# Kernel optimization log

Hardware: AMD Instinct MI355X
Metric: run time of the kernel (lower is better)

## Reference

```python
import jax, jax.numpy as jnp
import numpy as np

N = 16384       # structure nodes
H = 256         # in_channels == hidden_channels
E_BOLD = 524288
E_TEMP = 262144
T_ATTR = 107    # hardcoded in temporal_edge_proj Linear(107, hidden)
EPS = 1e-5


def layer_norm(x, g, b):
    m = x.mean(-1, keepdims=True)
    v = ((x - m) ** 2).mean(-1, keepdims=True)
    return (x - m) * jax.lax.rsqrt(v + EPS) * g + b


def gcn_conv(x, W, b, edge_index, edge_weight):
    """PyG GCNConv: add self-loops (weight 1), symmetric normalization,
    out_i = sum_j norm_ij * (x_j @ W) + b."""
    n = x.shape[0]
    loop = jnp.arange(n)
    row = jnp.concatenate([edge_index[0], loop])   # source
    col = jnp.concatenate([edge_index[1], loop])   # target
    w = jnp.concatenate([edge_weight, jnp.ones((n,), x.dtype)])
    deg = jax.ops.segment_sum(w, col, num_segments=n)
    dis = jnp.where(deg > 0, jax.lax.rsqrt(jnp.where(deg > 0, deg, 1.0)), 0.0)
    norm = dis[row] * w * dis[col]
    h = x @ W                                       # [n, H]
    out = jax.ops.segment_sum(norm[:, None] * h[row], col, num_segments=n)
    return out + b


def setup_inputs() -> dict:
    key = jax.random.key(0)
    ks = jax.random.split(key, 12)
    s = 1.0 / np.sqrt(H)
    return {
        "x_struct": jax.random.normal(ks[0], (N, H), jnp.float32),
        "bold_edge_index": jax.random.randint(ks[1], (2, E_BOLD), 0, N),
        "bold_edge_weight": jax.random.uniform(ks[2], (E_BOLD,), jnp.float32),
        "temp_edge_index": jax.random.randint(ks[3], (2, E_TEMP), 0, N),
        "temp_edge_attr": jax.random.normal(ks[4], (E_TEMP, T_ATTR), jnp.float32),
        "W_bold": jax.random.normal(ks[5], (H, H), jnp.float32) * s,
        "b_bold": jnp.zeros((H,), jnp.float32),
        "W_temp": jax.random.normal(ks[6], (H, H), jnp.float32) * s,
        "b_temp": jnp.zeros((H,), jnp.float32),
        "ln_struct_g": jnp.ones((H,), jnp.float32),
        "ln_struct_b": jnp.zeros((H,), jnp.float32),
        "ln_temp_g": jnp.ones((H,), jnp.float32),
        "ln_temp_b": jnp.zeros((H,), jnp.float32),
        "proj_w1": jax.random.normal(ks[7], (T_ATTR, H), jnp.float32) / np.sqrt(T_ATTR),
        "proj_b1": jnp.zeros((H,), jnp.float32),
        "proj_g": jnp.ones((H,), jnp.float32),
        "proj_beta": jnp.zeros((H,), jnp.float32),
        "proj_w2": jax.random.normal(ks[8], (H, 1), jnp.float32) * 0.01,
        "proj_b2": jnp.ones((1,), jnp.float32),  # keeps temporal edge weights > 0 (valid GCN norm)
    }


def reference(x_struct, bold_edge_index, bold_edge_weight, temp_edge_index,
              temp_edge_attr, W_bold, b_bold, W_temp, b_temp,
              ln_struct_g, ln_struct_b, ln_temp_g, ln_temp_b,
              proj_w1, proj_b1, proj_g, proj_beta, proj_w2, proj_b2):
    s0 = x_struct
    # bold GCN + residual + struct_norm + relu
    bold_out = gcn_conv(s0, W_bold, b_bold, bold_edge_index, bold_edge_weight)
    s = jax.nn.relu(layer_norm(bold_out + s0, ln_struct_g, ln_struct_b))
    # temporal edge-attr MLP -> scalar edge weight (temporal_dim == 1)
    h = jax.nn.relu(layer_norm(temp_edge_attr @ proj_w1 + proj_b1, proj_g, proj_beta))
    temp_w = (h @ proj_w2 + proj_b2)[:, 0]          # [E_TEMP]
    # temporal GCN + residual + temporal_norm + relu
    temporal_out = gcn_conv(s, W_temp, b_temp, temp_edge_index, temp_w)
    s = jax.nn.relu(layer_norm(temporal_out + s, ln_temp_g, ln_temp_b))
    # final residual to original features through struct_norm
    return layer_norm(s + s0, ln_struct_g, ln_struct_b)
```

## Files before the change

### kernel.cpp

```cpp
#include <hip/hip_runtime.h>

constexpr int kN  = 16384;
constexpr int kEB = 524288;
constexpr int kET = 262144;
constexpr int kTA = 107;
constexpr float kEps = 1e-5f;
#define HN 256

typedef __attribute__((ext_vector_type(8))) short short8;
typedef __attribute__((ext_vector_type(4))) float floatx4;
typedef unsigned short u16;
typedef unsigned int u32;

#define GLOAD_LDS16(gp, lp)                                                    \
  __builtin_amdgcn_global_load_lds(                                            \
      (const __attribute__((address_space(1))) u32*)(gp),                      \
      (__attribute__((address_space(3))) u32*)(lp), 16, 0, 0)

__device__ __forceinline__ u32 bf16rn(float f) {
  u32 u = __float_as_uint(f);
  return (u + 0x7FFFu + ((u >> 16) & 1u)) >> 16;
}
__device__ __forceinline__ u32 pack2(float a, float b) {
  return bf16rn(a) | (bf16rn(b) << 16);
}
__device__ __forceinline__ float bf2f(u32 v) {
  return __uint_as_float(v << 16);
}
__device__ __forceinline__ u32 cvtpk(float lo, float hi) {
  u32 r;
  asm("v_cvt_pk_bf16_f32 %0, %1, %2" : "=v"(r) : "v"(lo), "v"(hi));
  return r;
}
__device__ __forceinline__ void ub8(uint4 u, float* f) {
  f[0] = bf2f(u.x & 0xFFFF); f[1] = bf2f(u.x >> 16);
  f[2] = bf2f(u.y & 0xFFFF); f[3] = bf2f(u.y >> 16);
  f[4] = bf2f(u.z & 0xFFFF); f[5] = bf2f(u.z >> 16);
  f[6] = bf2f(u.w & 0xFFFF); f[7] = bf2f(u.w >> 16);
}
__device__ __forceinline__ u32 swz512(u32 b) { return b ^ (((b >> 9) & 7u) << 4); }

__global__ __launch_bounds__(256)
void k_pack(const float* __restrict__ w1, const float* __restrict__ Wb,
            const float* __restrict__ Wt, const float* __restrict__ b1,
            const float* __restrict__ pg, const float* __restrict__ pbeta,
            const float* __restrict__ w2, u16* __restrict__ pk1,
            u16* __restrict__ pkb, u16* __restrict__ pkt,
            float4* __restrict__ pp) {
  int idx = blockIdx.x * 256 + threadIdx.x;
  if (idx < 32768) {
    int e = idx & 7, lane = (idx >> 3) & 63, ct = (idx >> 9) & 15, kk = idx >> 13;
    int k = kk * 32 + (lane >> 4) * 8 + e, col = ct * 16 + (lane & 15);
    pk1[idx] = (u16)(k < kTA ? bf16rn(w1[(size_t)k * 256 + col]) : 0);
  } else if (idx < 163840) {
    int j = idx - 32768;
    const float* W = (j < 65536) ? Wb : Wt;
    u16* pk = (j < 65536) ? pkb : pkt;
    int t = j & 65535;
    int e = t & 7, lane = (t >> 3) & 63, ct = (t >> 9) & 15, kt = t >> 13;
    int k = kt * 32 + (lane >> 4) * 8 + e, col = ct * 16 + (lane & 15);
    pk[t] = (u16)bf16rn(W[(size_t)k * 256 + col]);
  } else if (idx < 163840 + 256) {
    int col = idx - 163840;
    pp[col] = make_float4(b1[col], pg[col], pbeta[col], w2[col]);
  }
}

__global__ __launch_bounds__(256)
void k_cvt(const float* __restrict__ in, u16* __restrict__ out) {
  size_t i = (size_t)(blockIdx.x * 256 + threadIdx.x) * 8;
  float4 a = *(const float4*)(in + i);
  float4 b = *(const float4*)(in + i + 4);
  uint4 o = make_uint4(pack2(a.x, a.y), pack2(a.z, a.w),
                       pack2(b.x, b.y), pack2(b.z, b.w));
  *(uint4*)(out + i) = o;
}

__global__ __launch_bounds__(256)
void k_edge_prep_both(const int* __restrict__ bcol, const float* __restrict__ bw,
                      const int* __restrict__ tcol, const float* __restrict__ tw,
                      float* __restrict__ deg_b, int* __restrict__ cnt_b,
                      float* __restrict__ deg_t, int* __restrict__ cnt_t) {
  int e = blockIdx.x * 256 + threadIdx.x;
  if (e < kEB) {
    int c = bcol[e];
    atomicAdd(&deg_b[c], bw[e]);
    atomicAdd(&cnt_b[c], 1);
  } else {
    int t = e - kEB;
    int c = tcol[t];
    atomicAdd(&deg_t[c], tw[t]);
    atomicAdd(&cnt_t[c], 1);
  }
}

__global__ __launch_bounds__(256)
void k_scan_both(const int* __restrict__ cnt_b, int* __restrict__ base_b,
                 int* __restrict__ cur_b, const float* __restrict__ deg_b,
                 float* __restrict__ dis_b, const int* __restrict__ cnt_t,
                 int* __restrict__ base_t, int* __restrict__ cur_t,
                 const float* __restrict__ deg_t, float* __restrict__ dis_t) {
  const int* cnt = blockIdx.x ? cnt_t : cnt_b;
  int* base = blockIdx.x ? base_t : base_b;
  int* cur  = blockIdx.x ? cur_t : cur_b;
  const float* deg = blockIdx.x ? deg_t : deg_b;
  float* dis = blockIdx.x ? dis_t : dis_b;
  __shared__ int part[256];
  int tid = threadIdx.x;
  int per = kN >> 8;
  int i0 = tid * per;
  int s = 0;
  for (int k = 0; k < per; ++k) s += cnt[i0 + k];
  part[tid] = s;
  __syncthreads();
  for (int off = 1; off < 256; off <<= 1) {
    int v = (tid >= off) ? part[tid - off] : 0;
    __syncthreads();
    part[tid] += v;
    __syncthreads();
  }
  int run = (tid == 0) ? 0 : part[tid - 1];
  for (int k = 0; k < per; ++k) {
    base[i0 + k] = run; cur[i0 + k] = run; run += cnt[i0 + k];
    float d = deg[i0 + k] + 1.0f;
    dis[i0 + k] = (d > 0.f) ? rsqrtf(d) : 0.f;
  }
  if (tid == 255) base[kN] = run;
}

__global__ __launch_bounds__(256)
void k_fill_both(const int* __restrict__ bei, const float* __restrict__ bw,
                 const float* __restrict__ dis_b, int* __restrict__ cur_b,
                 int2* __restrict__ csr_b, const int* __restrict__ tei,
                 const float* __restrict__ tw, const float* __restrict__ dis_t,
                 int* __restrict__ cur_t, int2* __restrict__ csr_t) {
  int e = blockIdx.x * 256 + threadIdx.x;
  if (e < kEB) {
    int r = bei[e], c = bei[kEB + e];
    float nrm = dis_b[r] * bw[e] * dis_b[c];
    int pos = atomicAdd(&cur_b[c], 1);
    csr_b[pos] = make_int2(r, __float_as_int(nrm));
  } else {
    int t = e - kEB;
    int r = tei[t], c = tei[kET + t];
    float nrm = dis_t[r] * tw[t] * dis_t[c];
    int pos = atomicAdd(&cur_t[c], 1);
    csr_t[pos] = make_int2(r, __float_as_int(nrm));
  }
}

__global__ __launch_bounds__(256)
void k_gemm_mfma(const u16* __restrict__ Ab, const u16* __restrict__ pkW,
                 u16* __restrict__ Cb) {
  __shared__ __align__(16) u16 Atile[32 * 256];
  int tid = threadIdx.x;
  int w = tid >> 6, lane = tid & 63, low4 = lane & 15, hi = lane >> 4;
  int row0 = blockIdx.x * 32;

  const char* asrc = (const char*)(Ab + (size_t)row0 * 256);
#pragma unroll
  for (int i = 0; i < 4; ++i) {
    u32 d = (u32)(((i * 4 + w) * 64 + lane) * 16);
    GLOAD_LDS16(asrc + swz512(d), (char*)Atile + (i * 4 + w) * 1024);
  }

  floatx4 acc[2][4];
#pragma unroll
  for (int rt = 0; rt < 2; ++rt)
#pragma unroll
    for (int nn = 0; nn < 4; ++nn) acc[rt][nn] = (floatx4){0.f, 0.f, 0.f, 0.f};

  __syncthreads();

#pragma unroll
  for (int kt = 0; kt < 8; ++kt) {
    short8 bfr[4];
    const u16* pw = pkW + ((size_t)(kt * 16 + w * 4) * 64 + lane) * 8;
#pragma unroll
    for (int nn = 0; nn < 4; ++nn) bfr[nn] = *(const short8*)(pw + nn * 512);
    short8 afr[2];
#pragma unroll
    for (int rt = 0; rt < 2; ++rt) {
      u32 p = (u32)((rt * 16 + low4) * 512 + (kt * 32 + hi * 8) * 2);
      afr[rt] = *(const short8*)((const char*)Atile + swz512(p));
    }
#pragma unroll
    for (int rt = 0; rt < 2; ++rt)
#pragma unroll
      for (int nn = 0; nn < 4; ++nn)
        acc[rt][nn] = __builtin_amdgcn_mfma_f32_16x16x32_bf16(afr[rt], bfr[nn],
                                                              acc[rt][nn], 0, 0, 0);
  }
#pragma unroll
  for (int rt = 0; rt < 2; ++rt)
#pragma unroll
    for (int nn = 0; nn < 4; ++nn)
#pragma unroll
      for (int j = 0; j < 4; ++j) {
        int row = row0 + rt * 16 + hi * 4 + j;
        int col = w * 64 + nn * 16 + low4;
        Cb[(size_t)row * 256 + col] = (u16)bf16rn(acc[rt][nn][j]);
      }
}

#define PROJ_TILES 4
__global__ __launch_bounds__(512)
void k_proj_mfma(const float* __restrict__ attr, const u16* __restrict__ pk1,
                 const float* __restrict__ b1, const float4* __restrict__ pp,
                 const float* __restrict__ b2, float* __restrict__ temp_w) {
  __shared__ __align__(16) u16 Btile[32768];
  int tid = threadIdx.x;
  int w = tid >> 6, lane = tid & 63, low4 = lane & 15, hi = lane >> 4;

#pragma unroll
  for (int it = 0; it < 8; ++it) {
    int chunk = it * 512 + tid;
    GLOAD_LDS16((const char*)pk1 + (size_t)chunk * 16,
                (char*)Btile + (it * 512 + w * 64) * 16);
  }

  auto buildA = [&](int t, short8* a) {
    int e0 = (blockIdx.x * PROJ_TILES + t) * 128 + w * 16;
    const float* rowp = attr + (size_t)(e0 + low4) * kTA;
#pragma unroll
    for (int kk = 0; kk < 4; ++kk) {
      int kb = kk * 32 + hi * 8;
      float v[8];
#pragma unroll
      for (int e = 0; e < 8; ++e)
        v[e] = (kk < 3 || kb + e < kTA) ? rowp[kb + e] : 0.f;
      union { short8 s8; uint4 u4; } fr;
      fr.u4 = make_uint4(cvtpk(v[0], v[1]), cvtpk(v[2], v[3]),
                         cvtpk(v[4], v[5]), cvtpk(v[6], v[7]));
      a[kk] = fr.s8;
    }
  };

  short8 a_cur[4];
  buildA(0, a_cur);
  float b2s = b2[0];

  __syncthreads();

#pragma unroll
  for (int t = 0; t < PROJ_TILES; ++t) {
    int e0 = (blockIdx.x * PROJ_TILES + t) * 128 + w * 16;

    short8 a_next[4];
    if (t + 1 < PROJ_TILES) buildA(t + 1, a_next);

    u32 hvpk[16][2];
    float s1[4] = {0.f, 0.f, 0.f, 0.f}, s2[4] = {0.f, 0.f, 0.f, 0.f};
#pragma unroll
    for (int nn = 0; nn < 16; ++nn) {
      floatx4 acc = (floatx4){0.f, 0.f, 0.f, 0.f};
#pragma unroll
      for (int kk = 0; kk < 4; ++kk) {
        short8 bfr = *(const short8*)(Btile + ((size_t)(kk * 16 + nn) * 64 + lane) * 8);
        acc = __builtin_amdgcn_mfma_f32_16x16x32_bf16(a_cur[kk], bfr, acc, 0, 0, 0);
      }
      float b1v = b1[nn * 16 + low4];
      float h0 = acc[0] + b1v, h1 = acc[1] + b1v, h2 = acc[2] + b1v, h3 = acc[3] + b1v;
      s1[0] += h0; s2[0] += h0 * h0;
      s1[1] += h1; s2[1] += h1 * h1;
      s1[2] += h2; s2[2] += h2 * h2;
      s1[3] += h3; s2[3] += h3 * h3;
      hvpk[nn][0] = cvtpk(h0, h1);
      hvpk[nn][1] = cvtpk(h2, h3);
    }

    float mean[4], inv[4];
#pragma unroll
    for (int j = 0; j < 4; ++j) {
#pragma unroll
      for (int m = 1; m < 16; m <<= 1) {
        s1[j] += __shfl_xor(s1[j], m, 64);
        s2[j] += __shfl_xor(s2[j], m, 64);
      }
      mean[j] = s1[j] * (1.f / 256);
      inv[j] = rsqrtf(s2[j] * (1.f / 256) - mean[j] * mean[j] + kEps);
    }

    float d[4] = {0.f, 0.f, 0.f, 0.f};
#pragma unroll
    for (int nn = 0; nn < 16; ++nn) {
      float4 p = pp[nn * 16 + low4];
      float h0 = bf2f(hvpk[nn][0] & 0xFFFF);
      float h1 = bf2f(hvpk[nn][0] >> 16);
      float h2 = bf2f(hvpk[nn][1] & 0xFFFF);
      float h3 = bf2f(hvpk[nn][1] >> 16);
      d[0] += fmaxf((h0 - mean[0]) * inv[0] * p.y + p.z, 0.f) * p.w;
      d[1] += fmaxf((h1 - mean[1]) * inv[1] * p.y + p.z, 0.f) * p.w;
      d[2] += fmaxf((h2 - mean[2]) * inv[2] * p.y + p.z, 0.f) * p.w;
      d[3] += fmaxf((h3 - mean[3]) * inv[3] * p.y + p.z, 0.f) * p.w;
    }
#pragma unroll
    for (int j = 0; j < 4; ++j) {
#pragma unroll
      for (int m = 1; m < 16; m <<= 1) d[j] += __shfl_xor(d[j], m, 64);
      if (low4 == 0) temp_w[e0 + hi * 4 + j] = d[j] + b2s;
    }

#pragma unroll
    for (int kk = 0; kk < 4; ++kk) a_cur[kk] = a_next[kk];
  }
}

template <int FINAL>
__global__ __launch_bounds__(256)
void k_agg_ln(const u16* __restrict__ h, const void* __restrict__ residv,
              const float* __restrict__ x0, const int2* __restrict__ csr,
              const int* __restrict__ basep, const float* __restrict__ dis,
              const float* __restrict__ bias, const float* __restrict__ g1,
              const float* __restrict__ b1, const float* __restrict__ g2,
              const float* __restrict__ b2, void* __restrict__ outv) {
  int tid = threadIdx.x;
  int sub = tid >> 5, lane = tid & 31;
  int node = blockIdx.x * 8 + sub;
  int c = lane * 8;
  const u16* hcol = h + c;
  float di = dis[node];
  float sl = di * di;
  float acc[8];
  {
    uint4 u = *(const uint4*)(hcol + (size_t)node * HN);
    float f[8]; ub8(u, f);
#pragma unroll
    for (int i = 0; i < 8; ++i) acc[i] = f[i] * sl;
  }
  int e0 = basep[node], e1 = basep[node + 1];
  int k = e0;
  for (; k + 4 <= e1; k += 4) {
    int2 p0 = csr[k], p1 = csr[k + 1], p2 = csr[k + 2], p3 = csr[k + 3];
    uint4 u0 = *(const uint4*)(hcol + (size_t)p0.x * HN);
    uint4 u1 = *(const uint4*)(hcol + (size_t)p1.x * HN);
    uint4 u2 = *(const uint4*)(hcol + (size_t)p2.x * HN);
    uint4 u3 = *(const uint4*)(hcol + (size_t)p3.x * HN);
    float n0 = __int_as_float(p0.y), n1 = __int_as_float(p1.y);
    float n2 = __int_as_float(p2.y), n3 = __int_as_float(p3.y);
    float f0[8], f1[8], f2[8], f3[8];
    ub8(u0, f0); ub8(u1, f1); ub8(u2, f2); ub8(u3, f3);
#pragma unroll
    for (int i = 0; i < 8; ++i)
      acc[i] += n0 * f0[i] + n1 * f1[i] + n2 * f2[i] + n3 * f3[i];
  }
  for (; k < e1; ++k) {
    int2 p = csr[k];
    uint4 u = *(const uint4*)(hcol + (size_t)p.x * HN);
    float nf = __int_as_float(p.y);
    float f[8]; ub8(u, f);
#pragma unroll
    for (int i = 0; i < 8; ++i) acc[i] += nf * f[i];
  }
  float v[8];
  {
    float4 b0 = *(const float4*)(bias + c);
    float4 b4 = *(const float4*)(bias + c + 4);
    float bb[8] = {b0.x, b0.y, b0.z, b0.w, b4.x, b4.y, b4.z, b4.w};
    float rr[8];
    if (!FINAL) {
      const float* rp = (const float*)residv + (size_t)node * HN + c;
      float4 r0 = *(const float4*)rp;
      float4 r4 = *(const float4*)(rp + 4);
      rr[0] = r0.x; rr[1] = r0.y; rr[2] = r0.z; rr[3] = r0.w;
      rr[4] = r4.x; rr[5] = r4.y; rr[6] = r4.z; rr[7] = r4.w;
    } else {
      uint4 u = *(const uint4*)((const u16*)residv + (size_t)node * HN + c);
      ub8(u, rr);
    }
#pragma unroll
    for (int i = 0; i < 8; ++i) v[i] = acc[i] + bb[i] + rr[i];
  }
  float s1 = 0.f, s2 = 0.f;
#pragma unroll
  for (int i = 0; i < 8; ++i) { s1 += v[i]; s2 += v[i] * v[i]; }
#pragma unroll
  for (int m = 1; m < 32; m <<= 1) {
    s1 += __shfl_xor(s1, m, 64);
    s2 += __shfl_xor(s2, m, 64);
  }
  float mean = s1 * (1.f / HN);
  float inv = rsqrtf(s2 * (1.f / HN) - mean * mean + kEps);
  float4 ga = *(const float4*)(g1 + c);
  float4 gb = *(const float4*)(g1 + c + 4);
  float4 ba = *(const float4*)(b1 + c);
  float4 bbv = *(const float4*)(b1 + c + 4);
  float gg[8] = {ga.x, ga.y, ga.z, ga.w, gb.x, gb.y, gb.z, gb.w};
  float bt[8] = {ba.x, ba.y, ba.z, ba.w, bbv.x, bbv.y, bbv.z, bbv.w};
  float y[8];
#pragma unroll
  for (int i = 0; i < 8; ++i)
    y[i] = fmaxf((v[i] - mean) * inv * gg[i] + bt[i], 0.f);
  if (!FINAL) {
    uint4 o = make_uint4(cvtpk(y[0], y[1]), cvtpk(y[2], y[3]),
                         cvtpk(y[4], y[5]), cvtpk(y[6], y[7]));
    *(uint4*)((u16*)outv + (size_t)node * HN + c) = o;
  } else {
    const float* xp = x0 + (size_t)node * HN + c;
    float4 x0v = *(const float4*)xp;
    float4 x4v = *(const float4*)(xp + 4);
    float xx[8] = {x0v.x, x0v.y, x0v.z, x0v.w, x4v.x, x4v.y, x4v.z, x4v.w};
    float z[8];
    float t1 = 0.f, t2 = 0.f;
#pragma unroll
    for (int i = 0; i < 8; ++i) {
      z[i] = y[i] + xx[i];
      t1 += z[i]; t2 += z[i] * z[i];
    }
#pragma unroll
    for (int m = 1; m < 32; m <<= 1) {
      t1 += __shfl_xor(t1, m, 64);
      t2 += __shfl_xor(t2, m, 64);
    }
    float m2 = t1 * (1.f / HN);
    float i2 = rsqrtf(t2 * (1.f / HN) - m2 * m2 + kEps);
    float4 Ga = *(const float4*)(g2 + c);
    float4 Gb = *(const float4*)(g2 + c + 4);
    float4 Ba = *(const float4*)(b2 + c);
    float4 Bb = *(const float4*)(b2 + c + 4);
    float G[8] = {Ga.x, Ga.y, Ga.z, Ga.w, Gb.x, Gb.y, Gb.z, Gb.w};
    float B[8] = {Ba.x, Ba.y, Ba.z, Ba.w, Bb.x, Bb.y, Bb.z, Bb.w};
    float* op = (float*)outv + (size_t)node * HN + c;
    float4 o0 = make_float4((z[0] - m2) * i2 * G[0] + B[0],
                            (z[1] - m2) * i2 * G[1] + B[1],
                            (z[2] - m2) * i2 * G[2] + B[2],
                            (z[3] - m2) * i2 * G[3] + B[3]);
    float4 o4 = make_float4((z[4] - m2) * i2 * G[4] + B[4],
                            (z[5] - m2) * i2 * G[5] + B[5],
                            (z[6] - m2) * i2 * G[6] + B[6],
                            (z[7] - m2) * i2 * G[7] + B[7]);
    *(float4*)op = o0;
    *(float4*)(op + 4) = o4;
  }
}

extern "C" void kernel_launch(void* const* d_in, const int* in_sizes, int n_in,
                              void* d_out, int out_size, void* d_ws, size_t ws_size,
                              hipStream_t stream) {
  const float* x     = (const float*)d_in[0];
  const int*   bei   = (const int*)d_in[1];
  const float* bew   = (const float*)d_in[2];
  const int*   tei   = (const int*)d_in[3];
  const float* tattr = (const float*)d_in[4];
  const float* Wb    = (const float*)d_in[5];
  const float* bb    = (const float*)d_in[6];
  const float* Wt    = (const float*)d_in[7];
  const float* bt    = (const float*)d_in[8];
  const float* gs    = (const float*)d_in[9];
  const float* bs    = (const float*)d_in[10];
  const float* gt    = (const float*)d_in[11];
  const float* btn   = (const float*)d_in[12];
  const float* pw1   = (const float*)d_in[13];
  const float* pb1   = (const float*)d_in[14];
  const float* pg    = (const float*)d_in[15];
  const float* pbeta = (const float*)d_in[16];
  const float* pw2   = (const float*)d_in[17];
  const float* pb2   = (const float*)d_in[18];
  float* outp = (float*)d_out;

  size_t off = 0;
  auto alloc = [&](size_t bytes) -> void* {
    void* p = (char*)d_ws + off;
    off += (bytes + 255) & ~(size_t)255;
    return p;
  };
  float* deg_b = (float*)alloc(kN * 4);
  float* deg_t = (float*)alloc(kN * 4);
  int*   cnt_b = (int*)alloc(kN * 4);
  int*   cnt_t = (int*)alloc(kN * 4);
  float* dis_b = (float*)alloc(kN * 4);
  float* dis_t = (float*)alloc(kN * 4);
  int*   base_b = (int*)alloc((kN + 1) * 4);
  int*   base_t = (int*)alloc((kN + 1) * 4);
  int*   cur_b  = (int*)alloc(kN * 4);
  int*   cur_t  = (int*)alloc(kN * 4);
  float* tmpw   = (float*)alloc(kET * 4);
  int2*  csr_b  = (int2*)alloc((size_t)kEB * 8);
  int2*  csr_t  = (int2*)alloc((size_t)kET * 8);
  u16*   pk1 = (u16*)alloc(32768 * 2);
  u16*   pkb = (u16*)alloc(65536 * 2);
  u16*   pkt = (u16*)alloc(65536 * 2);
  float4* pp = (float4*)alloc(256 * 16);
  u16*   xb  = (u16*)alloc((size_t)kN * HN * 2);
  u16*   hb  = (u16*)alloc((size_t)kN * HN * 2);
  u16*   sb  = (u16*)alloc((size_t)kN * HN * 2);
  (void)ws_size; (void)in_sizes; (void)n_in; (void)out_size;

  hipMemsetAsync(deg_b, 0, (size_t)4 * kN * 4, stream);

  k_pack<<<641, 256, 0, stream>>>(pw1, Wb, Wt, pb1, pg, pbeta, pw2,
                                  pk1, pkb, pkt, pp);
  k_cvt<<<kN * HN / 8 / 256, 256, 0, stream>>>(x, xb);

  k_proj_mfma<<<kET / 128 / PROJ_TILES, 512, 0, stream>>>(tattr, pk1, pb1, pp,
                                                          pb2, tmpw);

  k_edge_prep_both<<<(kEB + kET) / 256, 256, 0, stream>>>(
      bei + kEB, bew, tei + kET, tmpw, deg_b, cnt_b, deg_t, cnt_t);
  k_scan_both<<<2, 256, 0, stream>>>(cnt_b, base_b, cur_b, deg_b, dis_b,
                                     cnt_t, base_t, cur_t, deg_t, dis_t);
  k_fill_both<<<(kEB + kET) / 256, 256, 0, stream>>>(
      bei, bew, dis_b, cur_b, csr_b, tei, tmpw, dis_t, cur_t, csr_t);

  k_gemm_mfma<<<kN / 32, 256, 0, stream>>>(xb, pkb, hb);
  k_agg_ln<0><<<kN / 8, 256, 0, stream>>>(hb, x, nullptr, csr_b, base_b, dis_b,
                                          bb, gs, bs, nullptr, nullptr, sb);
  k_gemm_mfma<<<kN / 32, 256, 0, stream>>>(sb, pkt, hb);
  k_agg_ln<1><<<kN / 8, 256, 0, stream>>>(hb, sb, x, csr_t, base_t, dis_t,
                                          bt, gt, btn, gs, bs, outp);
}
```

Before: 270.4 us.

## Fuse independent stages into horizontally merged kernels to cut launches and overlap work

```diff
diff --git a/kernel.cpp b/kernel.cpp
--- a/kernel.cpp
+++ b/kernel.cpp
@@ -41,70 +41,202 @@
 __device__ __forceinline__ u32 swz512(u32 b) { return b ^ (((b >> 9) & 7u) << 4); }
 
 __global__ __launch_bounds__(256)
-void k_pack(const float* __restrict__ w1, const float* __restrict__ Wb,
-            const float* __restrict__ Wt, const float* __restrict__ b1,
-            const float* __restrict__ pg, const float* __restrict__ pbeta,
-            const float* __restrict__ w2, u16* __restrict__ pk1,
-            u16* __restrict__ pkb, u16* __restrict__ pkt,
-            float4* __restrict__ pp) {
-  int idx = blockIdx.x * 256 + threadIdx.x;
-  if (idx < 32768) {
-    int e = idx & 7, lane = (idx >> 3) & 63, ct = (idx >> 9) & 15, kk = idx >> 13;
-    int k = kk * 32 + (lane >> 4) * 8 + e, col = ct * 16 + (lane & 15);
-    pk1[idx] = (u16)(k < kTA ? bf16rn(w1[(size_t)k * 256 + col]) : 0);
-  } else if (idx < 163840) {
-    int j = idx - 32768;
-    const float* W = (j < 65536) ? Wb : Wt;
-    u16* pk = (j < 65536) ? pkb : pkt;
-    int t = j & 65535;
-    int e = t & 7, lane = (t >> 3) & 63, ct = (t >> 9) & 15, kt = t >> 13;
-    int k = kt * 32 + (lane >> 4) * 8 + e, col = ct * 16 + (lane & 15);
-    pk[t] = (u16)bf16rn(W[(size_t)k * 256 + col]);
-  } else if (idx < 163840 + 256) {
-    int col = idx - 163840;
-    pp[col] = make_float4(b1[col], pg[col], pbeta[col], w2[col]);
-  }
-}
-
-__global__ __launch_bounds__(256)
-void k_cvt(const float* __restrict__ in, u16* __restrict__ out) {
-  size_t i = (size_t)(blockIdx.x * 256 + threadIdx.x) * 8;
-  float4 a = *(const float4*)(in + i);
-  float4 b = *(const float4*)(in + i + 4);
-  uint4 o = make_uint4(pack2(a.x, a.y), pack2(a.z, a.w),
-                       pack2(b.x, b.y), pack2(b.z, b.w));
-  *(uint4*)(out + i) = o;
-}
-
-__global__ __launch_bounds__(256)
-void k_edge_prep_both(const int* __restrict__ bcol, const float* __restrict__ bw,
-                      const int* __restrict__ tcol, const float* __restrict__ tw,
-                      float* __restrict__ deg_b, int* __restrict__ cnt_b,
-                      float* __restrict__ deg_t, int* __restrict__ cnt_t) {
-  int e = blockIdx.x * 256 + threadIdx.x;
-  if (e < kEB) {
-    int c = bcol[e];
-    atomicAdd(&deg_b[c], bw[e]);
-    atomicAdd(&cnt_b[c], 1);
+void k_prep_const(const float* __restrict__ w1, const float* __restrict__ Wb,
+                  const float* __restrict__ Wt, const float* __restrict__ b1,
+                  const float* __restrict__ pg, const float* __restrict__ pbeta,
+                  const float* __restrict__ w2, u16* __restrict__ pk1,
+                  u16* __restrict__ pkb, u16* __restrict__ pkt,
+                  float4* __restrict__ pp, const float* __restrict__ x,
+                  u16* __restrict__ xb, uint4* __restrict__ zero4) {
+  int bid = blockIdx.x, tid = threadIdx.x;
+  if (bid < 641) {
+    int idx = bid * 256 + tid;
+    if (idx < 32768) {
+      int e = idx & 7, lane = (idx >> 3) & 63, ct = (idx >> 9) & 15, kk = idx >> 13;
+      int k = kk * 32 + (lane >> 4) * 8 + e, col = ct * 16 + (lane & 15);
+      pk1[idx] = (u16)(k < kTA ? bf16rn(w1[(size_t)k * 256 + col]) : 0);
+    } else if (idx < 163840) {
+      int j = idx - 32768;
+      const float* W = (j < 65536) ? Wb : Wt;
+      u16* pk = (j < 65536) ? pkb : pkt;
+      int t = j & 65535;
+      int e = t & 7, lane = (t >> 3) & 63, ct = (t >> 9) & 15, kt = t >> 13;
+      int k = kt * 32 + (lane >> 4) * 8 + e, col = ct * 16 + (lane & 15);
+      pk[t] = (u16)bf16rn(W[(size_t)k * 256 + col]);
+    } else if (idx < 163840 + 256) {
+      int col = idx - 163840;
+      pp[col] = make_float4(b1[col], pg[col], pbeta[col], w2[col]);
+    }
+  } else if (bid < 641 + 2048) {
+    size_t i = (size_t)((bid - 641) * 256 + tid) * 8;
+    float4 a = *(const float4*)(x + i);
+    float4 b = *(const float4*)(x + i + 4);
+    *(uint4*)(xb + i) = make_uint4(pack2(a.x, a.y), pack2(a.z, a.w),
+                                   pack2(b.x, b.y), pack2(b.z, b.w));
   } else {
-    int t = e - kEB;
-    int c = tcol[t];
-    atomicAdd(&deg_t[c], tw[t]);
-    atomicAdd(&cnt_t[c], 1);
-  }
-}
-
-__global__ __launch_bounds__(256)
-void k_scan_both(const int* __restrict__ cnt_b, int* __restrict__ base_b,
-                 int* __restrict__ cur_b, const float* __restrict__ deg_b,
-                 float* __restrict__ dis_b, const int* __restrict__ cnt_t,
-                 int* __restrict__ base_t, int* __restrict__ cur_t,
-                 const float* __restrict__ deg_t, float* __restrict__ dis_t) {
-  const int* cnt = blockIdx.x ? cnt_t : cnt_b;
-  int* base = blockIdx.x ? base_t : base_b;
-  int* cur  = blockIdx.x ? cur_t : cur_b;
-  const float* deg = blockIdx.x ? deg_t : deg_b;
-  float* dis = blockIdx.x ? dis_t : dis_b;
+    zero4[(bid - 2689) * 256 + tid] = make_uint4(0, 0, 0, 0);
+  }
+}
+
+#define PROJ_TILES 4
+__device__ __forceinline__
+void proj_role(u16* Btile, const float* __restrict__ attr,
+               const u16* __restrict__ pk1, const float* __restrict__ b1,
+               const float4* __restrict__ pp, const float* __restrict__ b2,
+               float* __restrict__ temp_w, int projid, int tid) {
+  int w = tid >> 6, lane = tid & 63, low4 = lane & 15, hi = lane >> 4;
+
+#pragma unroll
+  for (int it = 0; it < 8; ++it) {
+    int chunk = it * 512 + tid;
+    GLOAD_LDS16((const char*)pk1 + (size_t)chunk * 16,
+                (char*)Btile + (it * 512 + w * 64) * 16);
+  }
+
+  auto buildA = [&](int t, short8* a) {
+    int e0 = (projid * PROJ_TILES + t) * 128 + w * 16;
+    const float* rowp = attr + (size_t)(e0 + low4) * kTA;
+#pragma unroll
+    for (int kk = 0; kk < 4; ++kk) {
+      int kb = kk * 32 + hi * 8;
+      float v[8];
+#pragma unroll
+      for (int e = 0; e < 8; ++e)
+        v[e] = (kk < 3 || kb + e < kTA) ? rowp[kb + e] : 0.f;
+      union { short8 s8; uint4 u4; } fr;
+      fr.u4 = make_uint4(cvtpk(v[0], v[1]), cvtpk(v[2], v[3]),
+                         cvtpk(v[4], v[5]), cvtpk(v[6], v[7]));
+      a[kk] = fr.s8;
+    }
+  };
+
+  short8 a_cur[4];
+  buildA(0, a_cur);
+  float b2s = b2[0];
+
+  __syncthreads();
+
+#pragma unroll
+  for (int t = 0; t < PROJ_TILES; ++t) {
+    int e0 = (projid * PROJ_TILES + t) * 128 + w * 16;
+    short8 a_next[4];
+    if (t + 1 < PROJ_TILES) buildA(t + 1, a_next);
+
+    u32 hvpk[16][2];
+    float s1[4] = {0.f, 0.f, 0.f, 0.f}, s2[4] = {0.f, 0.f, 0.f, 0.f};
+#pragma unroll
+    for (int nn = 0; nn < 16; ++nn) {
+      floatx4 acc = (floatx4){0.f, 0.f, 0.f, 0.f};
+#pragma unroll
+      for (int kk = 0; kk < 4; ++kk) {
+        short8 bfr = *(const short8*)(Btile + ((size_t)(kk * 16 + nn) * 64 + lane) * 8);
+        acc = __builtin_amdgcn_mfma_f32_16x16x32_bf16(a_cur[kk], bfr, acc, 0, 0, 0);
+      }
+      float b1v = b1[nn * 16 + low4];
+      float h0 = acc[0] + b1v, h1 = acc[1] + b1v, h2 = acc[2] + b1v, h3 = acc[3] + b1v;
+      s1[0] += h0; s2[0] += h0 * h0;
+      s1[1] += h1; s2[1] += h1 * h1;
+      s1[2] += h2; s2[2] += h2 * h2;
+      s1[3] += h3; s2[3] += h3 * h3;
+      hvpk[nn][0] = cvtpk(h0, h1);
+      hvpk[nn][1] = cvtpk(h2, h3);
+    }
+
+    float mean[4], inv[4];
+#pragma unroll
+    for (int j = 0; j < 4; ++j) {
+#pragma unroll
+      for (int m = 1; m < 16; m <<= 1) {
+        s1[j] += __shfl_xor(s1[j], m, 64);
+        s2[j] += __shfl_xor(s2[j], m, 64);
+      }
+      mean[j] = s1[j] * (1.f / 256);
+      inv[j] = rsqrtf(s2[j] * (1.f / 256) - mean[j] * mean[j] + kEps);
+    }
+
+    float d[4] = {0.f, 0.f, 0.f, 0.f};
+#pragma unroll
+    for (int nn = 0; nn < 16; ++nn) {
+      float4 p = pp[nn * 16 + low4];
+      float h0 = bf2f(hvpk[nn][0] & 0xFFFF);
+      float h1 = bf2f(hvpk[nn][0] >> 16);
+      float h2 = bf2f(hvpk[nn][1] & 0xFFFF);
+      float h3 = bf2f(hvpk[nn][1] >> 16);
+      d[0] += fmaxf((h0 - mean[0]) * inv[0] * p.y + p.z, 0.f) * p.w;
+      d[1] += fmaxf((h1 - mean[1]) * inv[1] * p.y + p.z, 0.f) * p.w;
+      d[2] += fmaxf((h2 - mean[2]) * inv[2] * p.y + p.z, 0.f) * p.w;
+      d[3] += fmaxf((h3 - mean[3]) * inv[3] * p.y + p.z, 0.f) * p.w;
+    }
+#pragma unroll
+    for (int j = 0; j < 4; ++j) {
+#pragma unroll
+      for (int m = 1; m < 16; m <<= 1) d[j] += __shfl_xor(d[j], m, 64);
+      if (low4 == 0) temp_w[e0 + hi * 4 + j] = d[j] + b2s;
+    }
+#pragma unroll
+    for (int kk = 0; kk < 4; ++kk) a_cur[kk] = a_next[kk];
+  }
+}
+
+__device__ __forceinline__
+void gemm64_role(u16* shmem, const u16* __restrict__ Ab,
+                 const u16* __restrict__ pkW, u16* __restrict__ Cb,
+                 int gid, int tid) {
+  int half = tid >> 8, t = tid & 255;
+  int w = t >> 6, lane = t & 63, low4 = lane & 15, hi = lane >> 4;
+  int row0 = gid * 64 + half * 32;
+  u16* Atile = shmem + half * 8192;
+
+  const char* asrc = (const char*)(Ab + (size_t)row0 * 256);
+#pragma unroll
+  for (int i = 0; i < 4; ++i) {
+    u32 d = (u32)(((i * 4 + w) * 64 + lane) * 16);
+    GLOAD_LDS16(asrc + swz512(d), (char*)Atile + (i * 4 + w) * 1024);
+  }
+
+  floatx4 acc[2][4];
+#pragma unroll
+  for (int rt = 0; rt < 2; ++rt)
+#pragma unroll
+    for (int nn = 0; nn < 4; ++nn) acc[rt][nn] = (floatx4){0.f, 0.f, 0.f, 0.f};
+
+  __syncthreads();
+
+#pragma unroll
+  for (int kt = 0; kt < 8; ++kt) {
+    short8 bfr[4];
+    const u16* pw = pkW + ((size_t)(kt * 16 + w * 4) * 64 + lane) * 8;
+#pragma unroll
+    for (int nn = 0; nn < 4; ++nn) bfr[nn] = *(const short8*)(pw + nn * 512);
+    short8 afr[2];
+#pragma unroll
+    for (int rt = 0; rt < 2; ++rt) {
+      u32 p = (u32)((rt * 16 + low4) * 512 + (kt * 32 + hi * 8) * 2);
+      afr[rt] = *(const short8*)((const char*)Atile + swz512(p));
+    }
+#pragma unroll
+    for (int rt = 0; rt < 2; ++rt)
+#pragma unroll
+      for (int nn = 0; nn < 4; ++nn)
+        acc[rt][nn] = __builtin_amdgcn_mfma_f32_16x16x32_bf16(afr[rt], bfr[nn],
+                                                              acc[rt][nn], 0, 0, 0);
+  }
+#pragma unroll
+  for (int rt = 0; rt < 2; ++rt)
+#pragma unroll
+    for (int nn = 0; nn < 4; ++nn)
+#pragma unroll
+      for (int j = 0; j < 4; ++j) {
+        int row = row0 + rt * 16 + hi * 4 + j;
+        int col = w * 64 + nn * 16 + low4;
+        Cb[(size_t)row * 256 + col] = (u16)bf16rn(acc[rt][nn][j]);
+      }
+}
+
+__device__ __forceinline__
+void scan_role(const int* __restrict__ cnt, int* __restrict__ base,
+               int* __restrict__ cur, const float* __restrict__ deg,
+               float* __restrict__ dis) {
   __shared__ int part[256];
   int tid = threadIdx.x;
   int per = kN >> 8;
@@ -128,195 +260,17 @@
   if (tid == 255) base[kN] = run;
 }
 
-__global__ __launch_bounds__(256)
-void k_fill_both(const int* __restrict__ bei, const float* __restrict__ bw,
-                 const float* __restrict__ dis_b, int* __restrict__ cur_b,
-                 int2* __restrict__ csr_b, const int* __restrict__ tei,
-                 const float* __restrict__ tw, const float* __restrict__ dis_t,
-                 int* __restrict__ cur_t, int2* __restrict__ csr_t) {
-  int e = blockIdx.x * 256 + threadIdx.x;
-  if (e < kEB) {
-    int r = bei[e], c = bei[kEB + e];
-    float nrm = dis_b[r] * bw[e] * dis_b[c];
-    int pos = atomicAdd(&cur_b[c], 1);
-    csr_b[pos] = make_int2(r, __float_as_int(nrm));
-  } else {
-    int t = e - kEB;
-    int r = tei[t], c = tei[kET + t];
-    float nrm = dis_t[r] * tw[t] * dis_t[c];
-    int pos = atomicAdd(&cur_t[c], 1);
-    csr_t[pos] = make_int2(r, __float_as_int(nrm));
-  }
-}
-
-__global__ __launch_bounds__(256)
-void k_gemm_mfma(const u16* __restrict__ Ab, const u16* __restrict__ pkW,
-                 u16* __restrict__ Cb) {
-  __shared__ __align__(16) u16 Atile[32 * 256];
-  int tid = threadIdx.x;
-  int w = tid >> 6, lane = tid & 63, low4 = lane & 15, hi = lane >> 4;
-  int row0 = blockIdx.x * 32;
-
-  const char* asrc = (const char*)(Ab + (size_t)row0 * 256);
-#pragma unroll
-  for (int i = 0; i < 4; ++i) {
-    u32 d = (u32)(((i * 4 + w) * 64 + lane) * 16);
-    GLOAD_LDS16(asrc + swz512(d), (char*)Atile + (i * 4 + w) * 1024);
-  }
-
-  floatx4 acc[2][4];
-#pragma unroll
-  for (int rt = 0; rt < 2; ++rt)
-#pragma unroll
-    for (int nn = 0; nn < 4; ++nn) acc[rt][nn] = (floatx4){0.f, 0.f, 0.f, 0.f};
-
-  __syncthreads();
-
-#pragma unroll
-  for (int kt = 0; kt < 8; ++kt) {
-    short8 bfr[4];
-    const u16* pw = pkW + ((size_t)(kt * 16 + w * 4) * 64 + lane) * 8;
-#pragma unroll
-    for (int nn = 0; nn < 4; ++nn) bfr[nn] = *(const short8*)(pw + nn * 512);
-    short8 afr[2];
-#pragma unroll
-    for (int rt = 0; rt < 2; ++rt) {
-      u32 p = (u32)((rt * 16 + low4) * 512 + (kt * 32 + hi * 8) * 2);
-      afr[rt] = *(const short8*)((const char*)Atile + swz512(p));
-    }
-#pragma unroll
-    for (int rt = 0; rt < 2; ++rt)
-#pragma unroll
-      for (int nn = 0; nn < 4; ++nn)
-        acc[rt][nn] = __builtin_amdgcn_mfma_f32_16x16x32_bf16(afr[rt], bfr[nn],
-                                                              acc[rt][nn], 0, 0, 0);
-  }
-#pragma unroll
-  for (int rt = 0; rt < 2; ++rt)
-#pragma unroll
-    for (int nn = 0; nn < 4; ++nn)
-#pragma unroll
-      for (int j = 0; j < 4; ++j) {
-        int row = row0 + rt * 16 + hi * 4 + j;
-        int col = w * 64 + nn * 16 + low4;
-        Cb[(size_t)row * 256 + col] = (u16)bf16rn(acc[rt][nn][j]);
-      }
-}
-
-#define PROJ_TILES 4
-__global__ __launch_bounds__(512)
-void k_proj_mfma(const float* __restrict__ attr, const u16* __restrict__ pk1,
-                 const float* __restrict__ b1, const float4* __restrict__ pp,
-                 const float* __restrict__ b2, float* __restrict__ temp_w) {
-  __shared__ __align__(16) u16 Btile[32768];
-  int tid = threadIdx.x;
-  int w = tid >> 6, lane = tid & 63, low4 = lane & 15, hi = lane >> 4;
-
-#pragma unroll
-  for (int it = 0; it < 8; ++it) {
-    int chunk = it * 512 + tid;
-    GLOAD_LDS16((const char*)pk1 + (size_t)chunk * 16,
-                (char*)Btile + (it * 512 + w * 64) * 16);
-  }
-
-  auto buildA = [&](int t, short8* a) {
-    int e0 = (blockIdx.x * PROJ_TILES + t) * 128 + w * 16;
-    const float* rowp = attr + (size_t)(e0 + low4) * kTA;
-#pragma unroll
-    for (int kk = 0; kk < 4; ++kk) {
-      int kb = kk * 32 + hi * 8;
-      float v[8];
-#pragma unroll
-      for (int e = 0; e < 8; ++e)
-        v[e] = (kk < 3 || kb + e < kTA) ? rowp[kb + e] : 0.f;
-      union { short8 s8; uint4 u4; } fr;
-      fr.u4 = make_uint4(cvtpk(v[0], v[1]), cvtpk(v[2], v[3]),
-                         cvtpk(v[4], v[5]), cvtpk(v[6], v[7]));
-      a[kk] = fr.s8;
-    }
-  };
-
-  short8 a_cur[4];
-  buildA(0, a_cur);
-  float b2s = b2[0];
-
-  __syncthreads();
-
-#pragma unroll
-  for (int t = 0; t < PROJ_TILES; ++t) {
-    int e0 = (blockIdx.x * PROJ_TILES + t) * 128 + w * 16;
-
-    short8 a_next[4];
-    if (t + 1 < PROJ_TILES) buildA(t + 1, a_next);
-
-    u32 hvpk[16][2];
-    float s1[4] = {0.f, 0.f, 0.f, 0.f}, s2[4] = {0.f, 0.f, 0.f, 0.f};
-#pragma unroll
-    for (int nn = 0; nn < 16; ++nn) {
-      floatx4 acc = (floatx4){0.f, 0.f, 0.f, 0.f};
-#pragma unroll
-      for (int kk = 0; kk < 4; ++kk) {
-        short8 bfr = *(const short8*)(Btile + ((size_t)(kk * 16 + nn) * 64 + lane) * 8);
-        acc = __builtin_amdgcn_mfma_f32_16x16x32_bf16(a_cur[kk], bfr, acc, 0, 0, 0);
-      }
-      float b1v = b1[nn * 16 + low4];
-      float h0 = acc[0] + b1v, h1 = acc[1] + b1v, h2 = acc[2] + b1v, h3 = acc[3] + b1v;
-      s1[0] += h0; s2[0] += h0 * h0;
-      s1[1] += h1; s2[1] += h1 * h1;
-      s1[2] += h2; s2[2] += h2 * h2;
-      s1[3] += h3; s2[3] += h3 * h3;
-      hvpk[nn][0] = cvtpk(h0, h1);
-      hvpk[nn][1] = cvtpk(h2, h3);
-    }
-
-    float mean[4], inv[4];
-#pragma unroll
-    for (int j = 0; j < 4; ++j) {
-#pragma unroll
-      for (int m = 1; m < 16; m <<= 1) {
-        s1[j] += __shfl_xor(s1[j], m, 64);
-        s2[j] += __shfl_xor(s2[j], m, 64);
-      }
-      mean[j] = s1[j] * (1.f / 256);
-      inv[j] = rsqrtf(s2[j] * (1.f / 256) - mean[j] * mean[j] + kEps);
-    }
-
-    float d[4] = {0.f, 0.f, 0.f, 0.f};
-#pragma unroll
-    for (int nn = 0; nn < 16; ++nn) {
-      float4 p = pp[nn * 16 + low4];
-      float h0 = bf2f(hvpk[nn][0] & 0xFFFF);
-      float h1 = bf2f(hvpk[nn][0] >> 16);
-      float h2 = bf2f(hvpk[nn][1] & 0xFFFF);
-      float h3 = bf2f(hvpk[nn][1] >> 16);
-      d[0] += fmaxf((h0 - mean[0]) * inv[0] * p.y + p.z, 0.f) * p.w;
-      d[1] += fmaxf((h1 - mean[1]) * inv[1] * p.y + p.z, 0.f) * p.w;
-      d[2] += fmaxf((h2 - mean[2]) * inv[2] * p.y + p.z, 0.f) * p.w;
-      d[3] += fmaxf((h3 - mean[3]) * inv[3] * p.y + p.z, 0.f) * p.w;
-    }
-#pragma unroll
-    for (int j = 0; j < 4; ++j) {
-#pragma unroll
-      for (int m = 1; m < 16; m <<= 1) d[j] += __shfl_xor(d[j], m, 64);
-      if (low4 == 0) temp_w[e0 + hi * 4 + j] = d[j] + b2s;
-    }
-
-#pragma unroll
-    for (int kk = 0; kk < 4; ++kk) a_cur[kk] = a_next[kk];
-  }
-}
-
 template <int FINAL>
-__global__ __launch_bounds__(256)
-void k_agg_ln(const u16* __restrict__ h, const void* __restrict__ residv,
+__device__ __forceinline__
+void agg_role(const u16* __restrict__ h, const void* __restrict__ residv,
               const float* __restrict__ x0, const int2* __restrict__ csr,
               const int* __restrict__ basep, const float* __restrict__ dis,
               const float* __restrict__ bias, const float* __restrict__ g1,
               const float* __restrict__ b1, const float* __restrict__ g2,
-              const float* __restrict__ b2, void* __restrict__ outv) {
+              const float* __restrict__ b2, void* __restrict__ outv, int aid) {
   int tid = threadIdx.x;
   int sub = tid >> 5, lane = tid & 31;
-  int node = blockIdx.x * 8 + sub;
+  int node = aid * 8 + sub;
   int c = lane * 8;
   const u16* hcol = h + c;
   float di = dis[node];
@@ -421,17 +375,160 @@
     float G[8] = {Ga.x, Ga.y, Ga.z, Ga.w, Gb.x, Gb.y, Gb.z, Gb.w};
     float B[8] = {Ba.x, Ba.y, Ba.z, Ba.w, Bb.x, Bb.y, Bb.z, Bb.w};
     float* op = (float*)outv + (size_t)node * HN + c;
-    float4 o0 = make_float4((z[0] - m2) * i2 * G[0] + B[0],
-                            (z[1] - m2) * i2 * G[1] + B[1],
-                            (z[2] - m2) * i2 * G[2] + B[2],
-                            (z[3] - m2) * i2 * G[3] + B[3]);
-    float4 o4 = make_float4((z[4] - m2) * i2 * G[4] + B[4],
-                            (z[5] - m2) * i2 * G[5] + B[5],
-                            (z[6] - m2) * i2 * G[6] + B[6],
-                            (z[7] - m2) * i2 * G[7] + B[7]);
-    *(float4*)op = o0;
-    *(float4*)(op + 4) = o4;
-  }
+    *(float4*)op = make_float4((z[0] - m2) * i2 * G[0] + B[0],
+                               (z[1] - m2) * i2 * G[1] + B[1],
+                               (z[2] - m2) * i2 * G[2] + B[2],
+                               (z[3] - m2) * i2 * G[3] + B[3]);
+    *(float4*)(op + 4) = make_float4((z[4] - m2) * i2 * G[4] + B[4],
+                                     (z[5] - m2) * i2 * G[5] + B[5],
+                                     (z[6] - m2) * i2 * G[6] + B[6],
+                                     (z[7] - m2) * i2 * G[7] + B[7]);
+  }
+}
+
+__global__ __launch_bounds__(512)
+void k_uber1(const float* __restrict__ attr, const u16* __restrict__ pk1,
+             const float* __restrict__ b1, const float4* __restrict__ pp,
+             const float* __restrict__ b2, float* __restrict__ temp_w,
+             const u16* __restrict__ xb, const u16* __restrict__ pkb,
+             u16* __restrict__ hb, const int* __restrict__ bcol,
+             const float* __restrict__ bw, float* __restrict__ deg_b,
+             int* __restrict__ cnt_b) {
+  __shared__ __align__(16) u16 shmem[32768];
+  int bid = blockIdx.x, tid = threadIdx.x;
+  int r = bid >> 8, idx = bid & 255;
+  if (r == 0 || r == 2) {
+    proj_role(shmem, attr, pk1, b1, pp, b2, temp_w, idx + (r == 2 ? 256 : 0), tid);
+  } else if (r == 1) {
+    gemm64_role(shmem, xb, pkb, hb, idx, tid);
+  } else {
+    int eid = ((r - 3) * 256 + idx) * 512 + tid;
+    if (eid < kEB) {
+      int c = bcol[eid];
+      atomicAdd(&deg_b[c], bw[eid]);
+      atomicAdd(&cnt_b[c], 1);
+    }
+  }
+}
+
+__global__ __launch_bounds__(256)
+void k_scanb_prept(const int* __restrict__ cnt_b, int* __restrict__ base_b,
+                   int* __restrict__ cur_b, const float* __restrict__ deg_b,
+                   float* __restrict__ dis_b, const int* __restrict__ tcol,
+                   const float* __restrict__ tmpw, float* __restrict__ deg_t,
+                   int* __restrict__ cnt_t) {
+  if (blockIdx.x == 0) {
+    scan_role(cnt_b, base_b, cur_b, deg_b, dis_b);
+  } else {
+    int eid = (blockIdx.x - 1) * 256 + threadIdx.x;
+    int c = tcol[eid];
+    atomicAdd(&deg_t[c], tmpw[eid]);
+    atomicAdd(&cnt_t[c], 1);
+  }
+}
+
+__global__ __launch_bounds__(256)
+void k_fillb_scant(const int* __restrict__ bei, const float* __restrict__ bw,
+                   const float* __restrict__ dis_b, int* __restrict__ cur_b,
+                   int2* __restrict__ csr_b, const int* __restrict__ cnt_t,
+                   int* __restrict__ base_t, int* __restrict__ cur_t,
+                   const float* __restrict__ deg_t, float* __restrict__ dis_t) {
+  if (blockIdx.x == 0) {
+    scan_role(cnt_t, base_t, cur_t, deg_t, dis_t);
+  } else {
+    int eid = (blockIdx.x - 1) * 256 + threadIdx.x;
+    int rr = bei[eid], c = bei[kEB + eid];
+    float nrm = dis_b[rr] * bw[eid] * dis_b[c];
+    int pos = atomicAdd(&cur_b[c], 1);
+    csr_b[pos] = make_int2(rr, __float_as_int(nrm));
+  }
+}
+
+__global__ __launch_bounds__(256)
+void k_agg0_fillt(const u16* __restrict__ hb, const float* __restrict__ x,
+                  const int2* __restrict__ csr_b, const int* __restrict__ base_b,
+                  const float* __restrict__ dis_b, const float* __restrict__ bbias,
+                  const float* __restrict__ gs, const float* __restrict__ bs,
+                  u16* __restrict__ sb, const int* __restrict__ tei,
+                  const float* __restrict__ tmpw, const float* __restrict__ dis_t,
+                  int* __restrict__ cur_t, int2* __restrict__ csr_t) {
+  int bid = blockIdx.x;
+  int r = bid >> 8, idx = bid & 255;
+  if (r % 3 == 1) {
+    int eid = ((r / 3) * 256 + idx) * 256 + threadIdx.x;
+    int rr = tei[eid], c = tei[kET + eid];
+    float nrm = dis_t[rr] * tmpw[eid] * dis_t[c];
+    int pos = atomicAdd(&cur_t[c], 1);
+    csr_t[pos] = make_int2(rr, __float_as_int(nrm));
+  } else {
+    int agg_ord = r - r / 3 - (r % 3 == 2 ? 1 : 0);
+    agg_role<0>(hb, x, nullptr, csr_b, base_b, dis_b, bbias, gs, bs,
+                nullptr, nullptr, sb, agg_ord * 256 + idx);
+  }
+}
+
+__global__ __launch_bounds__(256)
+void k_gemm_mfma(const u16* __restrict__ Ab, const u16* __restrict__ pkW,
+                 u16* __restrict__ Cb) {
+  __shared__ __align__(16) u16 Atile[32 * 256];
+  int tid = threadIdx.x;
+  int w = tid >> 6, lane = tid & 63, low4 = lane & 15, hi = lane >> 4;
+  int row0 = blockIdx.x * 32;
+
+  const char* asrc = (const char*)(Ab + (size_t)row0 * 256);
+#pragma unroll
+  for (int i = 0; i < 4; ++i) {
+    u32 d = (u32)(((i * 4 + w) * 64 + lane) * 16);
+    GLOAD_LDS16(asrc + swz512(d), (char*)Atile + (i * 4 + w) * 1024);
+  }
+
+  floatx4 acc[2][4];
+#pragma unroll
+  for (int rt = 0; rt < 2; ++rt)
+#pragma unroll
+    for (int nn = 0; nn < 4; ++nn) acc[rt][nn] = (floatx4){0.f, 0.f, 0.f, 0.f};
+
+  __syncthreads();
+
+#pragma unroll
+  for (int kt = 0; kt < 8; ++kt) {
+    short8 bfr[4];
+    const u16* pw = pkW + ((size_t)(kt * 16 + w * 4) * 64 + lane) * 8;
+#pragma unroll
+    for (int nn = 0; nn < 4; ++nn) bfr[nn] = *(const short8*)(pw + nn * 512);
+    short8 afr[2];
+#pragma unroll
+    for (int rt = 0; rt < 2; ++rt) {
+      u32 p = (u32)((rt * 16 + low4) * 512 + (kt * 32 + hi * 8) * 2);
+      afr[rt] = *(const short8*)((const char*)Atile + swz512(p));
+    }
+#pragma unroll
+    for (int rt = 0; rt < 2; ++rt)
+#pragma unroll
+      for (int nn = 0; nn < 4; ++nn)
+        acc[rt][nn] = __builtin_amdgcn_mfma_f32_16x16x32_bf16(afr[rt], bfr[nn],
+                                                              acc[rt][nn], 0, 0, 0);
+  }
+#pragma unroll
+  for (int rt = 0; rt < 2; ++rt)
+#pragma unroll
+    for (int nn = 0; nn < 4; ++nn)
+#pragma unroll
+      for (int j = 0; j < 4; ++j) {
+        int row = row0 + rt * 16 + hi * 4 + j;
+        int col = w * 64 + nn * 16 + low4;
+        Cb[(size_t)row * 256 + col] = (u16)bf16rn(acc[rt][nn][j]);
+      }
+}
+
+__global__ __launch_bounds__(256)
+void k_agg1(const u16* __restrict__ h, const u16* __restrict__ sb,
+            const float* __restrict__ x0, const int2* __restrict__ csr,
+            const int* __restrict__ basep, const float* __restrict__ dis,
+            const float* __restrict__ bias, const float* __restrict__ g1,
+            const float* __restrict__ b1, const float* __restrict__ g2,
+            const float* __restrict__ b2, float* __restrict__ outp) {
+  agg_role<1>(h, sb, x0, csr, basep, dis, bias, g1, b1, g2, b2, outp, blockIdx.x);
 }
 
 extern "C" void kernel_launch(void* const* d_in, const int* in_sizes, int n_in,
@@ -486,26 +583,20 @@
   u16*   sb  = (u16*)alloc((size_t)kN * HN * 2);
   (void)ws_size; (void)in_sizes; (void)n_in; (void)out_size;
 
-  hipMemsetAsync(deg_b, 0, (size_t)4 * kN * 4, stream);
-
-  k_pack<<<641, 256, 0, stream>>>(pw1, Wb, Wt, pb1, pg, pbeta, pw2,
-                                  pk1, pkb, pkt, pp);
-  k_cvt<<<kN * HN / 8 / 256, 256, 0, stream>>>(x, xb);
-
-  k_proj_mfma<<<kET / 128 / PROJ_TILES, 512, 0, stream>>>(tattr, pk1, pb1, pp,
-                                                          pb2, tmpw);
-
-  k_edge_prep_both<<<(kEB + kET) / 256, 256, 0, stream>>>(
-      bei + kEB, bew, tei + kET, tmpw, deg_b, cnt_b, deg_t, cnt_t);
-  k_scan_both<<<2, 256, 0, stream>>>(cnt_b, base_b, cur_b, deg_b, dis_b,
-                                     cnt_t, base_t, cur_t, deg_t, dis_t);
-  k_fill_both<<<(kEB + kET) / 256, 256, 0, stream>>>(
-      bei, bew, dis_b, cur_b, csr_b, tei, tmpw, dis_t, cur_t, csr_t);
-
-  k_gemm_mfma<<<kN / 32, 256, 0, stream>>>(xb, pkb, hb);
-  k_agg_ln<0><<<kN / 8, 256, 0, stream>>>(hb, x, nullptr, csr_b, base_b, dis_b,
-                                          bb, gs, bs, nullptr, nullptr, sb);
+  k_prep_const<<<2753, 256, 0, stream>>>(pw1, Wb, Wt, pb1, pg, pbeta, pw2,
+                                         pk1, pkb, pkt, pp, x, xb,
+                                         (uint4*)deg_b);
+  k_uber1<<<1792, 512, 0, stream>>>(tattr, pk1, pb1, pp, pb2, tmpw,
+                                    xb, pkb, hb, bei + kEB, bew, deg_b, cnt_b);
+  k_scanb_prept<<<1 + kET / 256, 256, 0, stream>>>(cnt_b, base_b, cur_b, deg_b,
+                                                   dis_b, tei + kET, tmpw,
+                                                   deg_t, cnt_t);
+  k_fillb_scant<<<1 + kEB / 256, 256, 0, stream>>>(bei, bew, dis_b, cur_b, csr_b,
+                                                   cnt_t, base_t, cur_t,
+                                                   deg_t, dis_t);
+  k_agg0_fillt<<<3072, 256, 0, stream>>>(hb, x, csr_b, base_b, dis_b, bb, gs, bs,
+                                         sb, tei, tmpw, dis_t, cur_t, csr_t);
   k_gemm_mfma<<<kN / 32, 256, 0, stream>>>(sb, pkt, hb);
-  k_agg_ln<1><<<kN / 8, 256, 0, stream>>>(hb, sb, x, csr_t, base_t, dis_t,
-                                          bt, gt, btn, gs, bs, outp);
-}
+  k_agg1<<<kN / 8, 256, 0, stream>>>(hb, sb, x, csr_t, base_t, dis_t,
+                                     bt, gt, btn, gs, bs, outp);
+}
```

Result: slower. 367.0 us (+35.7%).
